# Performance work log

Measured on AMD Instinct MI355X. Metric: run time of the kernel, lower is better.

Reference implementation:

```python
import jax, jax.numpy as jnp
import numpy as np
from jax import lax

EMB = 128  # embed_length
R = 4      # CBAM reduction


def _mlp(v, w1, b1, w2, b2):
    # shared CAM MLP: [B,C] -> [B,C//r] -> [B,C]
    return jax.nn.relu(v @ w1.T + b1) @ w2.T + b2


def _cbam(x, w1, b1, w2, b2, sw):
    # channel attention (CAM)
    mx = jnp.max(x, axis=(2, 3))
    av = jnp.mean(x, axis=(2, 3))
    gate = jax.nn.sigmoid(_mlp(mx, w1, b1, w2, b2) + _mlp(av, w1, b1, w2, b2))
    y = gate[:, :, None, None] * x
    # spatial attention (SAM): 7x7 conv over [max, mean] channel maps
    smx = jnp.max(y, axis=1, keepdims=True)
    sav = jnp.mean(y, axis=1, keepdims=True)
    s = lax.conv_general_dilated(jnp.concatenate([smx, sav], axis=1), sw,
                                 window_strides=(1, 1), padding=[(3, 3), (3, 3)])
    y = jax.nn.sigmoid(s) * y
    return y + x  # residual as in CBAM.forward


def _neck(x, w, b):
    # 1x1 conv == channel GEMM
    return jnp.einsum('bchw,oc->bohw', x, w) + b[None, :, None, None]


def setup_inputs() -> dict:
    key = jax.random.key(0)
    ks = jax.random.split(key, 40)
    B = 32
    f32 = jnp.float32
    inp = {
        'xin0': jax.random.normal(ks[0], (B, 256, 80, 80), f32),
        'xin1': jax.random.normal(ks[1], (B, 512, 40, 40), f32),
        'xin2': jax.random.normal(ks[2], (B, 1024, 20, 20), f32),
        'yolo_outputs': jax.random.normal(ks[3], (B, 8400, 6), f32),
        'reid_idx': jax.random.randint(ks[4], (B, 100), 0, 8400, dtype=jnp.int32),
        # 1x1 neck convs
        'nw0': jax.random.normal(ks[5], (EMB, 256), f32) * 0.05,
        'nb0': jnp.zeros((EMB,), f32),
        'nw1': jax.random.normal(ks[6], (EMB, 512), f32) * 0.05,
        'nb1': jnp.zeros((EMB,), f32),
        'nw2': jax.random.normal(ks[7], (EMB, 1024), f32) * 0.05,
        'nb2': jnp.zeros((EMB,), f32),
    }
    h = EMB // R
    for i in range(3):
        k = jax.random.split(ks[10 + i], 5)
        inp[f'c{i}w1'] = jax.random.normal(k[0], (h, EMB), f32) * 0.05
        inp[f'c{i}b1'] = jnp.zeros((h,), f32)
        inp[f'c{i}w2'] = jax.random.normal(k[1], (EMB, h), f32) * 0.05
        inp[f'c{i}b2'] = jnp.zeros((EMB,), f32)
        inp[f'c{i}sw'] = jax.random.normal(k[2], (1, 2, 7, 7), f32) * 0.05
    return inp


def reference(xin0, xin1, xin2, yolo_outputs, reid_idx,
              nw0, nb0, nw1, nb1, nw2, nb2,
              c0w1, c0b1, c0w2, c0b2, c0sw,
              c1w1, c1b1, c1w2, c1b2, c1sw,
              c2w1, c2b1, c2w2, c2b2, c2sw):
    f0 = _cbam(_neck(xin0, nw0, nb0), c0w1, c0b1, c0w2, c0b2, c0sw)
    f1 = _cbam(_neck(xin1, nw1, nb1), c1w1, c1b1, c1w2, c1b2, c1sw)
    f2 = _cbam(_neck(xin2, nw2, nb2), c2w1, c2b1, c2w2, c2b2, c2sw)
    B, C = f0.shape[0], f0.shape[1]
    reid_feat = jnp.concatenate([f0.reshape(B, C, -1),
                                 f1.reshape(B, C, -1),
                                 f2.reshape(B, C, -1)], axis=2)  # [B, C, 8400]
    # ragged per-batch gather reid_feat[b, :, reid_idx[b]] then stack columns -> [B*K, C]
    emb = jax.vmap(lambda f, idx: f[:, idx].T)(reid_feat, reid_idx)  # [B, K, C]
    return (yolo_outputs, emb.reshape(-1, C))
```

## Files before the change

### kernel.cpp

```cpp
#include <hip/hip_runtime.h>
#include <hip/hip_bf16.h>

typedef __attribute__((ext_vector_type(8))) short bf16x8;
typedef __attribute__((ext_vector_type(4))) float f32x4;

#define EMB 128
#define NB 32

__device__ __forceinline__ unsigned short f2bf(float f) {
  unsigned u = __float_as_uint(f);
  u = u + 0x7FFFu + ((u >> 16) & 1u);
  return (unsigned short)(u >> 16);
}
__device__ __forceinline__ unsigned ordf(float f) {
  unsigned u = __float_as_uint(f);
  return (u & 0x80000000u) ? ~u : (u | 0x80000000u);
}
__device__ __forceinline__ float unordf(unsigned v) {
  unsigned u = (v & 0x80000000u) ? (v & 0x7FFFFFFFu) : ~v;
  return __uint_as_float(u);
}
__device__ __forceinline__ void gl_lds16(const float* g, float* l) {
  __builtin_amdgcn_global_load_lds(
      (const __attribute__((address_space(1))) void*)g,
      (__attribute__((address_space(3))) void*)l, 16, 0, 0);
}

__global__ __launch_bounds__(256) void wconv_kernel(
    const float* __restrict__ w0, const float* __restrict__ w1, const float* __restrict__ w2,
    unsigned short* __restrict__ o0, unsigned short* __restrict__ o1, unsigned short* __restrict__ o2)
{
  const int t = blockIdx.x * 256 + threadIdx.x;
  const float* w; unsigned short* o; int i;
  if (t < 32768)       { w = w0; o = o0; i = t; }
  else if (t < 98304)  { w = w1; o = o1; i = t - 32768; }
  else                 { w = w2; o = o2; i = t - 98304; }
  o[i] = f2bf(w[i]);
}

__global__ __launch_bounds__(256, 3) void neck_kernel(
    const float* __restrict__ x0, const float* __restrict__ x1, const float* __restrict__ x2,
    const unsigned short* __restrict__ wb0, const unsigned short* __restrict__ wb1, const unsigned short* __restrict__ wb2,
    const float* __restrict__ bias0, const float* __restrict__ bias1, const float* __restrict__ bias2,
    unsigned short* __restrict__ f0o, unsigned short* __restrict__ f1o, unsigned short* __restrict__ f2o,
    unsigned* __restrict__ gmax, float* __restrict__ gsum)
{
  __shared__ float xs[64 * 128];
  __shared__ unsigned smax[EMB];
  __shared__ float ssum[EMB];
  const int tid = threadIdx.x;
  if (tid < EMB) { smax[tid] = 0u; ssum[tid] = 0.f; }

  const int bid = blockIdx.x;
  int sidx, r, K, HW;
  const float* x; const unsigned short* wb; const float* bias; unsigned short* f;
  if (bid < 128)      { sidx = 2; r = bid;       x = x2; wb = wb2; bias = bias2; f = f2o; K = 1024; HW = 400;  }
  else if (bid < 544) { sidx = 1; r = bid - 128; x = x1; wb = wb1; bias = bias1; f = f1o; K = 512;  HW = 1600; }
  else                { sidx = 0; r = bid - 544; x = x0; wb = wb0; bias = bias0; f = f0o; K = 256;  HW = 6400; }
  const int tile = r / NB, b = r % NB;
  const int p0 = tile * 128;
  const int wv = tid >> 6, lane = tid & 63, q = lane >> 4, col = lane & 15;
  const float* __restrict__ xb = x + (size_t)b * K * HW;
  const int pw = p0 + wv * 32;

  f32x4 acc[2][8];
#pragma unroll
  for (int mt = 0; mt < 2; mt++)
#pragma unroll
    for (int nt = 0; nt < 8; nt++) acc[mt][nt] = (f32x4){0.f, 0.f, 0.f, 0.f};

  const int pofs = min(p0 + (lane & 31) * 4, HW - 4);
  const int lrow = lane >> 5;

  for (int k0 = 0; k0 < K; k0 += 64) {
    const float* gp0 = xb + (size_t)(k0 + wv * 16 + lrow) * HW + pofs;
    float* lp0 = &xs[(wv * 16) * 128];
#pragma unroll
    for (int i = 0; i < 8; i++)
      gl_lds16(gp0 + (size_t)(2 * i) * HW, lp0 + (2 * i) * 128);
    __syncthreads();

#pragma unroll
    for (int kk = 0; kk < 2; kk++) {
      const int rb = kk * 32 + q * 8;
      float av0[8], av1[8];
#pragma unroll
      for (int j = 0; j < 8; j++) {
        av0[j] = xs[(rb + j) * 128 + (wv * 32) + col];
        av1[j] = xs[(rb + j) * 128 + (wv * 32) + 16 + col];
      }
      bf16x8 A0, A1;
#pragma unroll
      for (int j = 0; j < 8; j++) { A0[j] = (short)f2bf(av0[j]); A1[j] = (short)f2bf(av1[j]); }
      const int cg = k0 + rb;
#pragma unroll
      for (int nt = 0; nt < 8; nt++) {
        const bf16x8 B = *(const bf16x8*)(wb + (size_t)(nt * 16 + col) * K + cg);
        acc[0][nt] = __builtin_amdgcn_mfma_f32_16x16x32_bf16(A0, B, acc[0][nt], 0, 0, 0);
        acc[1][nt] = __builtin_amdgcn_mfma_f32_16x16x32_bf16(A1, B, acc[1][nt], 0, 0, 0);
      }
    }
    __syncthreads();
  }

#pragma unroll
  for (int nt = 0; nt < 8; nt++) {
    const int o = nt * 16 + col;
    const float bo = bias[o];
    float lmax = -3.4e38f, lsum = 0.f;
#pragma unroll
    for (int mt = 0; mt < 2; mt++) {
#pragma unroll
      for (int rr = 0; rr < 4; rr++) {
        const int p = pw + mt * 16 + q * 4 + rr;
        const float v = acc[mt][nt][rr] + bo;
        if (p < HW) {
          f[((size_t)b * HW + p) * EMB + o] = f2bf(v);
          lmax = fmaxf(lmax, v);
          lsum += v;
        }
      }
    }
#pragma unroll
    for (int off = 16; off < 64; off <<= 1) {
      lmax = fmaxf(lmax, __shfl_xor(lmax, off, 64));
      lsum += __shfl_xor(lsum, off, 64);
    }
    if (lane < 16) {
      atomicMax(&smax[o], ordf(lmax));
      atomicAdd(&ssum[o], lsum);
    }
  }
  __syncthreads();
  if (tid < EMB) {
    atomicMax(&gmax[(sidx * NB + b) * EMB + tid], smax[tid]);
    atomicAdd(&gsum[(sidx * NB + b) * EMB + tid], ssum[tid]);
  }
}

__global__ __launch_bounds__(128) void gate_kernel(
    const unsigned* __restrict__ gmax, const float* __restrict__ gsum, float* __restrict__ gate,
    const float* __restrict__ w1a, const float* __restrict__ b1a, const float* __restrict__ w2a, const float* __restrict__ b2a,
    const float* __restrict__ w1b, const float* __restrict__ b1b, const float* __restrict__ w2b, const float* __restrict__ b2b,
    const float* __restrict__ w1c, const float* __restrict__ b1c, const float* __restrict__ w2c, const float* __restrict__ b2c)
{
  const int s = blockIdx.y, b = blockIdx.x, tid = threadIdx.x;
  const float* w1 = s == 0 ? w1a : (s == 1 ? w1b : w1c);
  const float* b1 = s == 0 ? b1a : (s == 1 ? b1b : b1c);
  const float* w2 = s == 0 ? w2a : (s == 1 ? w2b : w2c);
  const float* b2 = s == 0 ? b2a : (s == 1 ? b2b : b2c);
  const float invHW = s == 0 ? (1.f / 6400.f) : (s == 1 ? (1.f / 1600.f) : (1.f / 400.f));
  __shared__ float mx[EMB], av[EMB], hm[32], ha[32];
  const int base = (s * NB + b) * EMB;
  mx[tid] = unordf(gmax[base + tid]);
  av[tid] = gsum[base + tid] * invHW;
  __syncthreads();
  if (tid < 32) {
    float sm = b1[tid], sa = b1[tid];
    for (int c = 0; c < EMB; c++) { const float wv = w1[tid * EMB + c]; sm += wv * mx[c]; sa += wv * av[c]; }
    hm[tid] = fmaxf(sm, 0.f); ha[tid] = fmaxf(sa, 0.f);
  }
  __syncthreads();
  float v = 2.f * b2[tid];
  for (int h = 0; h < 32; h++) { const float wv = w2[tid * 32 + h]; v += wv * (hm[h] + ha[h]); }
  gate[base + tid] = 1.f / (1.f + __expf(-v));
}

__global__ __launch_bounds__(256) void smap_kernel(
    const unsigned short* __restrict__ f0, const unsigned short* __restrict__ f1, const unsigned short* __restrict__ f2,
    const float* __restrict__ gate,
    float* __restrict__ smx0, float* __restrict__ sav0,
    float* __restrict__ smx1, float* __restrict__ sav1,
    float* __restrict__ smx2, float* __restrict__ sav2)
{
  const int lane = threadIdx.x & 63;
  const int wid = (blockIdx.x * blockDim.x + threadIdx.x) >> 6;
  const int nw = (gridDim.x * blockDim.x) >> 6;
  const int total = NB * 8400;
  for (int t = wid; t < total; t += nw) {
    const int b = t / 8400, p = t % 8400;
    const unsigned short* f; float* smx; float* sav; int s, pp, HW;
    if (p < 6400)      { s = 0; pp = p;        HW = 6400; f = f0; smx = smx0; sav = sav0; }
    else if (p < 8000) { s = 1; pp = p - 6400; HW = 1600; f = f1; smx = smx1; sav = sav1; }
    else               { s = 2; pp = p - 8000; HW = 400;  f = f2; smx = smx2; sav = sav2; }
    const unsigned u = ((const unsigned*)(f + ((size_t)b * HW + pp) * EMB))[lane];
    const float v0 = __uint_as_float(u << 16);
    const float v1 = __uint_as_float(u & 0xFFFF0000u);
    const int gb = (s * NB + b) * EMB + 2 * lane;
    const float y0 = gate[gb] * v0, y1 = gate[gb + 1] * v1;
    float m = fmaxf(y0, y1), sm = y0 + y1;
#pragma unroll
    for (int off = 1; off < 64; off <<= 1) { m = fmaxf(m, __shfl_xor(m, off, 64)); sm += __shfl_xor(sm, off, 64); }
    if (lane == 0) { smx[b * HW + pp] = m; sav[b * HW + pp] = sm * (1.f / EMB); }
  }
}

__global__ __launch_bounds__(256) void gather_kernel(
    const int* __restrict__ reid_idx,
    const unsigned short* __restrict__ f0, const unsigned short* __restrict__ f1, const unsigned short* __restrict__ f2,
    const float* __restrict__ gate,
    const float* __restrict__ smx0, const float* __restrict__ sav0,
    const float* __restrict__ smx1, const float* __restrict__ sav1,
    const float* __restrict__ smx2, const float* __restrict__ sav2,
    const float* __restrict__ sw0, const float* __restrict__ sw1, const float* __restrict__ sw2,
    float* __restrict__ emb)
{
  const int lane = threadIdx.x & 63;
  const int wid = (blockIdx.x * blockDim.x + threadIdx.x) >> 6;
  if (wid >= NB * 100) return;
  const int b = wid / 100, k = wid % 100;
  const int idx = reid_idx[b * 100 + k];
  const unsigned short* f; const float* smx; const float* sav; const float* sw;
  int s, pp, W, H, HW;
  if (idx < 6400)      { s = 0; pp = idx;        W = 80; H = 80; HW = 6400; f = f0; smx = smx0; sav = sav0; sw = sw0; }
  else if (idx < 8000) { s = 1; pp = idx - 6400; W = 40; H = 40; HW = 1600; f = f1; smx = smx1; sav = sav1; sw = sw1; }
  else                 { s = 2; pp = idx - 8000; W = 20; H = 20; HW = 400;  f = f2; smx = smx2; sav = sav2; sw = sw2; }
  const int y = pp / W, xx0 = pp % W;
  float c = 0.f;
  if (lane < 49) {
    const int dy = lane / 7 - 3, dx = lane % 7 - 3;
    const int yy = y + dy, xx = xx0 + dx;
    if (yy >= 0 && yy < H && xx >= 0 && xx < W) {
      const int qq = b * HW + yy * W + xx;
      c = smx[qq] * sw[lane] + sav[qq] * sw[49 + lane];
    }
  }
#pragma unroll
  for (int off = 1; off < 64; off <<= 1) c += __shfl_xor(c, off, 64);
  const float sig = 1.f / (1.f + __expf(-c));
  const unsigned u = ((const unsigned*)(f + ((size_t)b * HW + pp) * EMB))[lane];
  const float v0 = __uint_as_float(u << 16);
  const float v1 = __uint_as_float(u & 0xFFFF0000u);
  const int gb = (s * NB + b) * EMB + 2 * lane;
  const float o0 = v0 * (1.f + sig * gate[gb]);
  const float o1 = v1 * (1.f + sig * gate[gb + 1]);
  *(float2*)(emb + ((size_t)(b * 100 + k)) * EMB + 2 * lane) = make_float2(o0, o1);
}

extern "C" void kernel_launch(void* const* d_in, const int* in_sizes, int n_in,
                              void* d_out, int out_size, void* d_ws, size_t ws_size,
                              hipStream_t stream)
{
  const float* xin0 = (const float*)d_in[0];
  const float* xin1 = (const float*)d_in[1];
  const float* xin2 = (const float*)d_in[2];
  const float* yolo = (const float*)d_in[3];
  const int*   reid = (const int*)d_in[4];
  const float* nw0 = (const float*)d_in[5];  const float* nb0 = (const float*)d_in[6];
  const float* nw1 = (const float*)d_in[7];  const float* nb1 = (const float*)d_in[8];
  const float* nw2 = (const float*)d_in[9];  const float* nb2 = (const float*)d_in[10];
  const float* c0w1 = (const float*)d_in[11]; const float* c0b1 = (const float*)d_in[12];
  const float* c0w2 = (const float*)d_in[13]; const float* c0b2 = (const float*)d_in[14];
  const float* c0sw = (const float*)d_in[15];
  const float* c1w1 = (const float*)d_in[16]; const float* c1b1 = (const float*)d_in[17];
  const float* c1w2 = (const float*)d_in[18]; const float* c1b2 = (const float*)d_in[19];
  const float* c1sw = (const float*)d_in[20];
  const float* c2w1 = (const float*)d_in[21]; const float* c2b1 = (const float*)d_in[22];
  const float* c2w2 = (const float*)d_in[23]; const float* c2b2 = (const float*)d_in[24];
  const float* c2sw = (const float*)d_in[25];

  char* ws = (char*)d_ws;
  size_t off = 0;
  auto alloc = [&](size_t bytes) -> void* {
    void* p = ws + off; off += (bytes + 255) & ~(size_t)255; return p;
  };
  unsigned short* f0 = (unsigned short*)alloc((size_t)NB * 6400 * EMB * 2);
  unsigned short* f1 = (unsigned short*)alloc((size_t)NB * 1600 * EMB * 2);
  unsigned short* f2 = (unsigned short*)alloc((size_t)NB * 400 * EMB * 2);
  unsigned* gmax = (unsigned*)alloc(3 * NB * EMB * 4);
  float* gsum = (float*)alloc(3 * NB * EMB * 4);
  float* gate = (float*)alloc(3 * NB * EMB * 4);
  float* smx0 = (float*)alloc((size_t)NB * 6400 * 4);
  float* sav0 = (float*)alloc((size_t)NB * 6400 * 4);
  float* smx1 = (float*)alloc((size_t)NB * 1600 * 4);
  float* sav1 = (float*)alloc((size_t)NB * 1600 * 4);
  float* smx2 = (float*)alloc((size_t)NB * 400 * 4);
  float* sav2 = (float*)alloc((size_t)NB * 400 * 4);
  unsigned short* wb0 = (unsigned short*)alloc(32768 * 2);
  unsigned short* wb1 = (unsigned short*)alloc(65536 * 2);
  unsigned short* wb2 = (unsigned short*)alloc(131072 * 2);

  hipMemsetAsync(gmax, 0, (size_t)2 * 3 * NB * EMB * 4, stream);
  hipMemcpyAsync(d_out, yolo, (size_t)NB * 8400 * 6 * 4, hipMemcpyDeviceToDevice, stream);

  wconv_kernel<<<dim3(896), dim3(256), 0, stream>>>(nw0, nw1, nw2, wb0, wb1, wb2);

  neck_kernel<<<dim3(2144), dim3(256), 0, stream>>>(
      xin0, xin1, xin2, wb0, wb1, wb2, nb0, nb1, nb2, f0, f1, f2, gmax, gsum);

  gate_kernel<<<dim3(NB, 3), dim3(128), 0, stream>>>(gmax, gsum, gate,
      c0w1, c0b1, c0w2, c0b2, c1w1, c1b1, c1w2, c1b2, c2w1, c2b1, c2w2, c2b2);

  smap_kernel<<<dim3(4200), dim3(256), 0, stream>>>(f0, f1, f2, gate, smx0, sav0, smx1, sav1, smx2, sav2);

  gather_kernel<<<dim3(800), dim3(256), 0, stream>>>(reid, f0, f1, f2, gate,
      smx0, sav0, smx1, sav1, smx2, sav2, c0sw, c1sw, c2sw,
      (float*)d_out + (size_t)NB * 8400 * 6);
}
```

Measured before the change: 581.1 us.

## Double-buffer per-wave LDS staging in neck GEMM and fold memset/copy into kernels

```diff
diff --git a/kernel.cpp b/kernel.cpp
--- a/kernel.cpp
+++ b/kernel.cpp
@@ -7,10 +7,9 @@
 #define EMB 128
 #define NB 32
 
-__device__ __forceinline__ unsigned short f2bf(float f) {
-  unsigned u = __float_as_uint(f);
-  u = u + 0x7FFFu + ((u >> 16) & 1u);
-  return (unsigned short)(u >> 16);
+__device__ __forceinline__ short f2bf(float f) {
+  __bf16 h = (__bf16)f;
+  return __builtin_bit_cast(short, h);
 }
 __device__ __forceinline__ unsigned ordf(float f) {
   unsigned u = __float_as_uint(f);
@@ -28,28 +27,31 @@
 
 __global__ __launch_bounds__(256) void wconv_kernel(
     const float* __restrict__ w0, const float* __restrict__ w1, const float* __restrict__ w2,
-    unsigned short* __restrict__ o0, unsigned short* __restrict__ o1, unsigned short* __restrict__ o2)
+    unsigned short* __restrict__ o0, unsigned short* __restrict__ o1, unsigned short* __restrict__ o2,
+    unsigned* __restrict__ stats)
 {
   const int t = blockIdx.x * 256 + threadIdx.x;
+  if (t < 24576) stats[t] = 0u;
   const float* w; unsigned short* o; int i;
   if (t < 32768)       { w = w0; o = o0; i = t; }
   else if (t < 98304)  { w = w1; o = o1; i = t - 32768; }
   else                 { w = w2; o = o2; i = t - 98304; }
-  o[i] = f2bf(w[i]);
-}
-
-__global__ __launch_bounds__(256, 3) void neck_kernel(
+  o[i] = (unsigned short)f2bf(w[i]);
+}
+
+__global__ __launch_bounds__(256, 4) void neck_kernel(
     const float* __restrict__ x0, const float* __restrict__ x1, const float* __restrict__ x2,
     const unsigned short* __restrict__ wb0, const unsigned short* __restrict__ wb1, const unsigned short* __restrict__ wb2,
     const float* __restrict__ bias0, const float* __restrict__ bias1, const float* __restrict__ bias2,
     unsigned short* __restrict__ f0o, unsigned short* __restrict__ f1o, unsigned short* __restrict__ f2o,
     unsigned* __restrict__ gmax, float* __restrict__ gsum)
 {
-  __shared__ float xs[64 * 128];
+  __shared__ float xs[4][2][32 * 32];
   __shared__ unsigned smax[EMB];
   __shared__ float ssum[EMB];
   const int tid = threadIdx.x;
   if (tid < EMB) { smax[tid] = 0u; ssum[tid] = 0.f; }
+  __syncthreads();
 
   const int bid = blockIdx.x;
   int sidx, r, K, HW;
@@ -58,10 +60,14 @@
   else if (bid < 544) { sidx = 1; r = bid - 128; x = x1; wb = wb1; bias = bias1; f = f1o; K = 512;  HW = 1600; }
   else                { sidx = 0; r = bid - 544; x = x0; wb = wb0; bias = bias0; f = f0o; K = 256;  HW = 6400; }
   const int tile = r / NB, b = r % NB;
-  const int p0 = tile * 128;
   const int wv = tid >> 6, lane = tid & 63, q = lane >> 4, col = lane & 15;
+  const int pw = tile * 128 + wv * 32;
   const float* __restrict__ xb = x + (size_t)b * K * HW;
-  const int pw = p0 + wv * 32;
+
+  const int sg_row = lane >> 3;
+  const int sg_off = min(pw + (lane & 7) * 4, HW - 4);
+  float* buf0 = xs[wv][0];
+  float* buf1 = xs[wv][1];
 
   f32x4 acc[2][8];
 #pragma unroll
@@ -69,39 +75,40 @@
 #pragma unroll
     for (int nt = 0; nt < 8; nt++) acc[mt][nt] = (f32x4){0.f, 0.f, 0.f, 0.f};
 
-  const int pofs = min(p0 + (lane & 31) * 4, HW - 4);
-  const int lrow = lane >> 5;
-
+#define STAGE(kb, l) do {                                             \
+    const float* _g = xb + (size_t)((kb) + sg_row) * HW + sg_off;     \
+    _Pragma("unroll")                                                 \
+    for (int _i = 0; _i < 4; _i++)                                    \
+      gl_lds16(_g + (size_t)(8 * _i) * HW, (l) + _i * 256);           \
+  } while (0)
+
+#define COMPUTE(kg, l) do {                                           \
+    float av0[8], av1[8];                                             \
+    _Pragma("unroll")                                                 \
+    for (int _j = 0; _j < 8; _j++) {                                  \
+      av0[_j] = (l)[(q * 8 + _j) * 32 + col];                         \
+      av1[_j] = (l)[(q * 8 + _j) * 32 + col + 16];                    \
+    }                                                                 \
+    bf16x8 A0, A1;                                                    \
+    _Pragma("unroll")                                                 \
+    for (int _j = 0; _j < 8; _j++) { A0[_j] = f2bf(av0[_j]); A1[_j] = f2bf(av1[_j]); } \
+    _Pragma("unroll")                                                 \
+    for (int _nt = 0; _nt < 8; _nt++) {                               \
+      const bf16x8 B = *(const bf16x8*)(wb + (size_t)(_nt * 16 + col) * K + (kg) + q * 8); \
+      acc[0][_nt] = __builtin_amdgcn_mfma_f32_16x16x32_bf16(A0, B, acc[0][_nt], 0, 0, 0); \
+      acc[1][_nt] = __builtin_amdgcn_mfma_f32_16x16x32_bf16(A1, B, acc[1][_nt], 0, 0, 0); \
+    }                                                                 \
+  } while (0)
+
+  STAGE(0, buf0);
   for (int k0 = 0; k0 < K; k0 += 64) {
-    const float* gp0 = xb + (size_t)(k0 + wv * 16 + lrow) * HW + pofs;
-    float* lp0 = &xs[(wv * 16) * 128];
-#pragma unroll
-    for (int i = 0; i < 8; i++)
-      gl_lds16(gp0 + (size_t)(2 * i) * HW, lp0 + (2 * i) * 128);
-    __syncthreads();
-
-#pragma unroll
-    for (int kk = 0; kk < 2; kk++) {
-      const int rb = kk * 32 + q * 8;
-      float av0[8], av1[8];
-#pragma unroll
-      for (int j = 0; j < 8; j++) {
-        av0[j] = xs[(rb + j) * 128 + (wv * 32) + col];
-        av1[j] = xs[(rb + j) * 128 + (wv * 32) + 16 + col];
-      }
-      bf16x8 A0, A1;
-#pragma unroll
-      for (int j = 0; j < 8; j++) { A0[j] = (short)f2bf(av0[j]); A1[j] = (short)f2bf(av1[j]); }
-      const int cg = k0 + rb;
-#pragma unroll
-      for (int nt = 0; nt < 8; nt++) {
-        const bf16x8 B = *(const bf16x8*)(wb + (size_t)(nt * 16 + col) * K + cg);
-        acc[0][nt] = __builtin_amdgcn_mfma_f32_16x16x32_bf16(A0, B, acc[0][nt], 0, 0, 0);
-        acc[1][nt] = __builtin_amdgcn_mfma_f32_16x16x32_bf16(A1, B, acc[1][nt], 0, 0, 0);
-      }
-    }
-    __syncthreads();
-  }
+    STAGE(k0 + 32, buf1);
+    COMPUTE(k0, buf0);
+    if (k0 + 64 < K) STAGE(k0 + 64, buf0);
+    COMPUTE(k0 + 32, buf1);
+  }
+#undef STAGE
+#undef COMPUTE
 
 #pragma unroll
   for (int nt = 0; nt < 8; nt++) {
@@ -115,7 +122,7 @@
         const int p = pw + mt * 16 + q * 4 + rr;
         const float v = acc[mt][nt][rr] + bo;
         if (p < HW) {
-          f[((size_t)b * HW + p) * EMB + o] = f2bf(v);
+          f[((size_t)b * HW + p) * EMB + o] = (unsigned short)f2bf(v);
           lmax = fmaxf(lmax, v);
           lsum += v;
         }
@@ -235,6 +242,13 @@
   const float o0 = v0 * (1.f + sig * gate[gb]);
   const float o1 = v1 * (1.f + sig * gate[gb + 1]);
   *(float2*)(emb + ((size_t)(b * 100 + k)) * EMB + 2 * lane) = make_float2(o0, o1);
+}
+
+__global__ __launch_bounds__(256) void ycopy_kernel(
+    const float4* __restrict__ src, float4* __restrict__ dst, int n)
+{
+  const int i = blockIdx.x * 256 + threadIdx.x;
+  if (i < n) dst[i] = src[i];
 }
 
 extern "C" void kernel_launch(void* const* d_in, const int* in_sizes, int n_in,
@@ -280,10 +294,7 @@
   unsigned short* wb1 = (unsigned short*)alloc(65536 * 2);
   unsigned short* wb2 = (unsigned short*)alloc(131072 * 2);
 
-  hipMemsetAsync(gmax, 0, (size_t)2 * 3 * NB * EMB * 4, stream);
-  hipMemcpyAsync(d_out, yolo, (size_t)NB * 8400 * 6 * 4, hipMemcpyDeviceToDevice, stream);
-
-  wconv_kernel<<<dim3(896), dim3(256), 0, stream>>>(nw0, nw1, nw2, wb0, wb1, wb2);
+  wconv_kernel<<<dim3(896), dim3(256), 0, stream>>>(nw0, nw1, nw2, wb0, wb1, wb2, gmax);
 
   neck_kernel<<<dim3(2144), dim3(256), 0, stream>>>(
       xin0, xin1, xin2, wb0, wb1, wb2, nb0, nb1, nb2, f0, f1, f2, gmax, gsum);
@@ -296,4 +307,7 @@
   gather_kernel<<<dim3(800), dim3(256), 0, stream>>>(reid, f0, f1, f2, gate,
       smx0, sav0, smx1, sav1, smx2, sav2, c0sw, c1sw, c2sw,
       (float*)d_out + (size_t)NB * 8400 * 6);
-}
+
+  ycopy_kernel<<<dim3((NB * 8400 * 6 / 4 + 255) / 256), dim3(256), 0, stream>>>(
+      (const float4*)yolo, (float4*)d_out, NB * 8400 * 6 / 4);
+}
```

Result: no change. 572.7 us (-1.4%).
